# Optimization experiments

Measured on AMD Instinct MI355X. Metric: run time of the kernel, lower is better.

Reference implementation:

```python
import jax, jax.numpy as jnp
import numpy as np

CODEBOOK_SIZE = 1024
EMB_DIM = 64


def setup_inputs() -> dict:
    key = jax.random.key(0)
    k1, k2 = jax.random.split(key)
    z = jax.random.normal(k1, (4, EMB_DIM, 32, 32, 32), dtype=jnp.float32)
    embedding = jax.random.normal(k2, (CODEBOOK_SIZE, EMB_DIM), dtype=jnp.float32)
    return {"z": z, "embedding": embedding}


def reference(z, embedding):
    # z: [b, c, h, w, d], embedding: [K, c]
    b, c, h, w, d = z.shape
    K = embedding.shape[0]
    # flatten to [N, c] with channels last (matches permute(0,2,3,4,1).reshape)
    zf = jnp.transpose(z, (0, 2, 3, 4, 1)).reshape(-1, c)
    # squared L2 distance to each codebook entry: ||z||^2 - 2 z.e + ||e||^2
    dist = (
        jnp.sum(zf * zf, axis=1, keepdims=True)
        - 2.0 * zf @ embedding.T
        + jnp.sum(embedding * embedding, axis=1)[None, :]
    )  # [N, K]
    min_encoding_indices = jnp.argmin(dist, axis=1)  # [N]
    # one-hot @ embedding == gather (same math, no NxK materialization)
    z_q = embedding[min_encoding_indices]  # [N, c]
    z_q = jnp.transpose(z_q.reshape(b, h, w, d, c), (0, 4, 1, 2, 3))
    # straight-through estimator
    z_q = z + jax.lax.stop_gradient(z_q - z)
    # perplexity from mean one-hot occupancy
    n_tokens = zf.shape[0]
    e_mean = jnp.bincount(min_encoding_indices, length=K).astype(zf.dtype) / n_tokens
    perplexity = jnp.exp(-jnp.sum(e_mean * jnp.log(e_mean + 1e-10)))
    loss = jnp.asarray(0.0, dtype=z.dtype)
    return (
        z_q,
        loss,
        perplexity,
        min_encoding_indices.reshape(b, h, w, d),
        jnp.mean(dist),
    )
```

## Files before the change

kernel.cpp:

```cpp
#include <hip/hip_runtime.h>

#define CH     64
#define KC     1024
#define SP     32768
#define NBATCH 4
#define NTOK   (NBATCH * SP)
#define MTOK   64
#define SZZ    68
#define ECH    256
#define SZEB   72
#define CAP    16
#define MARGIN 3.0f

#define OFF_ZQ   0
#define OFF_LOSS (NBATCH * CH * SP)
#define OFF_PERP (OFF_LOSS + 1)
#define OFF_IDX  (OFF_PERP + 1)
#define OFF_MEAN (OFF_IDX + NTOK)


typedef __attribute__((ext_vector_type(8))) short  s16x8;
typedef __attribute__((ext_vector_type(4))) float  f32x4;

__device__ __forceinline__ unsigned short f2bf(float f) {
    unsigned int u = __float_as_uint(f);
    return (unsigned short)((u + 0x7fffu + ((u >> 16) & 1u)) >> 16);
}

__device__ __forceinline__ float exact_dist(const float* zrow,
                                            const float* __restrict__ emb,
                                            const float* enl, int c) {
    const float4* er = (const float4*)(emb + (size_t)c * CH);
    float a0 = 0.f, a1 = 0.f, a2 = 0.f, a3 = 0.f;
#pragma unroll
    for (int j = 0; j < 16; ++j) {
        float4 e4 = er[j];
        a0 = fmaf(zrow[4 * j + 0], e4.x, a0);
        a1 = fmaf(zrow[4 * j + 1], e4.y, a1);
        a2 = fmaf(zrow[4 * j + 2], e4.z, a2);
        a3 = fmaf(zrow[4 * j + 3], e4.w, a3);
    }
    return enl[c] - 2.f * ((a0 + a1) + (a2 + a3));
}

__global__ __launch_bounds__(256) void prep(const float* __restrict__ e,
                                            int* __restrict__ hist,
                                            float* __restrict__ sums,
                                            float* __restrict__ sum_zc,
                                            float* __restrict__ sum_ec,
                                            float* __restrict__ enorm,
                                            unsigned short* __restrict__ eb) {
    const int tid = threadIdx.x;
    const int bk = blockIdx.x;
    if (bk < 4) {
        int k = bk * 256 + tid;
        const float4* row = (const float4*)(e + (size_t)k * CH);
        float n = 0.f;
#pragma unroll
        for (int j = 0; j < CH / 4; ++j) {
            float4 v = row[j];
            n += v.x * v.x + v.y * v.y + v.z * v.z + v.w * v.w;
        }
        enorm[k] = n;
    } else if (bk == 4) {
        if (tid == 0) sums[0] = 0.f;
        if (tid < 64) sum_zc[tid] = 0.f;
        __shared__ float ls1[256];
        __shared__ float r2[4];
        int c = tid & 63;
        int strip = tid >> 6;
        float s1 = 0.f, s2 = 0.f;
        for (int k = strip * 256; k < strip * 256 + 256; ++k) {
            float v = e[k * CH + c];
            s1 += v;
            s2 = fmaf(v, v, s2);
        }
        ls1[tid] = s1;
        for (int off = 32; off; off >>= 1) s2 += __shfl_down(s2, off);
        if ((tid & 63) == 0) r2[tid >> 6] = s2;
        __syncthreads();
        if (strip == 0) sum_ec[c] = ls1[c] + ls1[64 + c] + ls1[128 + c] + ls1[192 + c];
        if (tid == 0) sums[1] = r2[0] + r2[1] + r2[2] + r2[3];
    } else if (bk < 9) {
        hist[(bk - 5) * 256 + tid] = 0;
    } else {
        int base = (bk - 9) * 16384;
        for (int j = 0; j < 64; ++j) {
            int i = base + tid + j * 256;
            eb[i] = f2bf(e[i]);
        }
    }
}

__global__ __launch_bounds__(256, 2) void vq_main(const float* __restrict__ z,
                                                  const float* __restrict__ emb,
                                                  const unsigned short* __restrict__ eb,
                                                  const float* __restrict__ enorm,
                                                  float* __restrict__ out,
                                                  int* __restrict__ hist,
                                                  float* __restrict__ sums,
                                                  float* __restrict__ sum_zc) {
    __shared__ float zl[MTOK * SZZ];
    __shared__ unsigned short ebl[ECH * SZEB];
    __shared__ float enorm_l[KC];
    __shared__ float dmin_l[MTOK];
    __shared__ float zs1[256], zs2[256];
    __shared__ int   cand[MTOK][CAP];
    __shared__ int   ccnt[MTOK];
    __shared__ int   fi[MTOK];

    const int tid = threadIdx.x;
    const int w = tid >> 6;
    const int lane = tid & 63;
    const int n15 = lane & 15;
    const int q = lane >> 4;
    const int t0 = blockIdx.x * MTOK;
    const int bb = t0 >> 15;
    const int s0 = t0 & (SP - 1);

    {
        const float* zbase = z + ((size_t)bb * CH) * SP + s0;
#pragma unroll
        for (int j = 0; j < 4; ++j) {
            int idx = tid + j * 256;
            int c = idx >> 4;
            int tq = idx & 15;
            float4 v = *(const float4*)(zbase + (size_t)c * SP + tq * 4);
            zl[(4 * tq + 0) * SZZ + c] = v.x;
            zl[(4 * tq + 1) * SZZ + c] = v.y;
            zl[(4 * tq + 2) * SZZ + c] = v.z;
            zl[(4 * tq + 3) * SZZ + c] = v.w;
        }
#pragma unroll
        for (int j = 0; j < 4; ++j) enorm_l[tid + j * 256] = enorm[tid + j * 256];
        if (tid < MTOK) ccnt[tid] = 0;
    }
    __syncthreads();

    s16x8 A0, A1;
    {
        const float* zrow = &zl[(w * 16 + n15) * SZZ];
        float4 za = *(const float4*)(zrow + q * 8);
        float4 zb = *(const float4*)(zrow + q * 8 + 4);
        float4 zc = *(const float4*)(zrow + 32 + q * 8);
        float4 zd = *(const float4*)(zrow + 32 + q * 8 + 4);
        A0[0] = (short)f2bf(za.x); A0[1] = (short)f2bf(za.y);
        A0[2] = (short)f2bf(za.z); A0[3] = (short)f2bf(za.w);
        A0[4] = (short)f2bf(zb.x); A0[5] = (short)f2bf(zb.y);
        A0[6] = (short)f2bf(zb.z); A0[7] = (short)f2bf(zb.w);
        A1[0] = (short)f2bf(zc.x); A1[1] = (short)f2bf(zc.y);
        A1[2] = (short)f2bf(zc.z); A1[3] = (short)f2bf(zc.w);
        A1[4] = (short)f2bf(zd.x); A1[5] = (short)f2bf(zd.y);
        A1[6] = (short)f2bf(zd.z); A1[7] = (short)f2bf(zd.w);
    }
    const unsigned short* ebq = ebl + (size_t)n15 * SZEB + q * 8;

    float bmin[4] = {3.4e38f, 3.4e38f, 3.4e38f, 3.4e38f};
    for (int ch = 0; ch < 4; ++ch) {
        __syncthreads();
#pragma unroll
        for (int rep = 0; rep < 8; ++rep) {
            int i = tid + rep * 256;
            int row = i >> 3, j = i & 7;
            ((float4*)&ebl[row * SZEB])[j] =
                ((const float4*)(eb + (size_t)(ch * ECH + row) * CH))[j];
        }
        __syncthreads();
        for (int ct = 0; ct < 16; ++ct) {
            const unsigned short* p = ebq + ct * 16 * SZEB;
            s16x8 B0 = *(const s16x8*)p;
            s16x8 B1 = *(const s16x8*)(p + 32);
            f32x4 acc = {0.f, 0.f, 0.f, 0.f};
            acc = __builtin_amdgcn_mfma_f32_16x16x32_bf16(A0, B0, acc, 0, 0, 0);
            acc = __builtin_amdgcn_mfma_f32_16x16x32_bf16(A1, B1, acc, 0, 0, 0);
            float en = enorm_l[ch * ECH + ct * 16 + n15];
#pragma unroll
            for (int r = 0; r < 4; ++r) {
                float d = fmaf(-2.f, acc[r], en);
                bmin[r] = fminf(bmin[r], d);
            }
        }
    }
#pragma unroll
    for (int off = 1; off < 16; off <<= 1)
#pragma unroll
        for (int r = 0; r < 4; ++r)
            bmin[r] = fminf(bmin[r], __shfl_xor(bmin[r], off));
    if (n15 == 0)
#pragma unroll
        for (int r = 0; r < 4; ++r) dmin_l[w * 16 + 4 * q + r] = bmin[r];
    __syncthreads();

    float thr[4];
#pragma unroll
    for (int r = 0; r < 4; ++r) thr[r] = dmin_l[w * 16 + 4 * q + r] + MARGIN;
    for (int cc = 0; cc < 4; ++cc) {
        int ch = (cc == 0) ? 3 : (cc - 1);
        if (cc) {
            __syncthreads();
#pragma unroll
            for (int rep = 0; rep < 8; ++rep) {
                int i = tid + rep * 256;
                int row = i >> 3, j = i & 7;
                ((float4*)&ebl[row * SZEB])[j] =
                    ((const float4*)(eb + (size_t)(ch * ECH + row) * CH))[j];
            }
            __syncthreads();
        }
        for (int ct = 0; ct < 16; ++ct) {
            const unsigned short* p = ebq + ct * 16 * SZEB;
            s16x8 B0 = *(const s16x8*)p;
            s16x8 B1 = *(const s16x8*)(p + 32);
            f32x4 acc = {0.f, 0.f, 0.f, 0.f};
            acc = __builtin_amdgcn_mfma_f32_16x16x32_bf16(A0, B0, acc, 0, 0, 0);
            acc = __builtin_amdgcn_mfma_f32_16x16x32_bf16(A1, B1, acc, 0, 0, 0);
            float en = enorm_l[ch * ECH + ct * 16 + n15];
#pragma unroll
            for (int r = 0; r < 4; ++r) {
                float d = fmaf(-2.f, acc[r], en);
                if (d <= thr[r]) {
                    int t = w * 16 + 4 * q + r;
                    int pos = atomicAdd(&ccnt[t], 1);
                    if (pos < CAP) cand[t][pos] = ch * ECH + ct * 16 + n15;
                }
            }
        }
    }
    __syncthreads();

    if (tid < MTOK) {
        int t = tid;
        const float* zrow = &zl[t * SZZ];
        int cnt = ccnt[t];
        float best = 3.4e38f;
        int bi = 0;
        if (cnt <= CAP) {
            for (int j = 0; j < cnt; ++j) {
                int c = cand[t][j];
                float d = exact_dist(zrow, emb, enorm_l, c);
                if (d < best || (d == best && c < bi)) { best = d; bi = c; }
            }
        } else {
            for (int c = 0; c < KC; ++c) {
                float d = exact_dist(zrow, emb, enorm_l, c);
                if (d < best) { best = d; bi = c; }
            }
        }
        fi[t] = bi;
        out[OFF_IDX + t0 + t] = (float)bi;
        atomicAdd(&hist[bi], 1);
    }
    __syncthreads();

#pragma unroll
    for (int j = 0; j < 16; ++j) {
        int idx = tid + j * 256;
        int c = idx >> 6;
        int t = idx & 63;
        int code = fi[t];
        float ev = emb[(size_t)code * CH + c];
        float zv = zl[t * SZZ + c];
        out[OFF_ZQ + ((size_t)bb * CH + c) * SP + s0 + t] = zv + (ev - zv);
    }

    {
        int c = tid >> 2, qq = tid & 3;
        float s1 = 0.f, s2 = 0.f;
        for (int tt = 0; tt < 16; ++tt) {
            float v = zl[(qq * 16 + tt) * SZZ + c];
            s1 += v;
            s2 = fmaf(v, v, s2);
        }
        zs1[tid] = s1;
        zs2[tid] = s2;
    }
    __syncthreads();
    if (tid < 64) {
        float a = zs1[4 * tid] + zs1[4 * tid + 1] + zs1[4 * tid + 2] + zs1[4 * tid + 3];
        atomicAdd(&sum_zc[tid], a);
        float bsum = zs2[4 * tid] + zs2[4 * tid + 1] + zs2[4 * tid + 2] + zs2[4 * tid + 3];
        for (int off = 32; off; off >>= 1) bsum += __shfl_down(bsum, off);
        if (tid == 0) atomicAdd(&sums[0], bsum);
    }
}

__global__ __launch_bounds__(1024) void finalize(const int* __restrict__ hist,
                                                 const float* __restrict__ sums,
                                                 const float* __restrict__ sum_zc,
                                                 const float* __restrict__ sum_ec,
                                                 float* __restrict__ out) {
    __shared__ float red[1024];
    int k = threadIdx.x;
    float p = (float)hist[k] * (1.0f / (float)NTOK);
    red[k] = p * logf(p + 1e-10f);
    __syncthreads();
    for (int off = 512; off; off >>= 1) {
        if (k < off) red[k] += red[k + off];
        __syncthreads();
    }
    if (k == 0) {
        out[OFF_PERP] = expf(-red[0]);
        out[OFF_LOSS] = 0.f;
        double dot = 0.0;
        for (int c = 0; c < CH; ++c) dot += (double)sum_zc[c] * (double)sum_ec[c];
        double mean = ((double)KC * (double)sums[0] + (double)NTOK * (double)sums[1] - 2.0 * dot)
                      / ((double)NTOK * (double)KC);
        out[OFF_MEAN] = (float)mean;
    }
}

extern "C" void kernel_launch(void* const* d_in, const int* in_sizes, int n_in,
                              void* d_out, int out_size, void* d_ws, size_t ws_size,
                              hipStream_t stream) {
    const float* z   = (const float*)d_in[0];
    const float* emb = (const float*)d_in[1];
    float* out = (float*)d_out;

    int*            hist   = (int*)d_ws;
    float*          sums   = (float*)d_ws + 1024;
    float*          sum_zc = (float*)d_ws + 1026;
    float*          sum_ec = (float*)d_ws + 1090;
    float*          enorm  = (float*)d_ws + 1154;
    unsigned short* eb     = (unsigned short*)((int*)d_ws + 4096);

    prep<<<13, 256, 0, stream>>>(emb, hist, sums, sum_zc, sum_ec, enorm, eb);
    vq_main<<<NTOK / MTOK, 256, 0, stream>>>(z, emb, eb, enorm, out, hist, sums, sum_zc);
    finalize<<<1, 1024, 0, stream>>>(hist, sums, sum_zc, sum_ec, out);
}
```

Before: 227.7 us.

## Enlarge token tile, fuse codebook prep and finalize into the main kernel

Each block now handles 256 tokens instead of 64. Each wave keeps four bf16 A-fragments in registers and reuses every codebook B-fragment across them, so codebook LDS traffic per token drops. The separate prep and finalize kernels are removed: each block computes codebook norms and bf16 conversion itself, and the last block, chosen with an atomic ticket, computes perplexity and the mean distance. The exact rescoring and z_q write read z back from global into registers. The z sums for the mean are now taken from bf16-rounded values, which lowers their precision, and every block repeats the codebook norm computation.

```diff
diff --git a/kernel.cpp b/kernel.cpp
--- a/kernel.cpp
+++ b/kernel.cpp
@@ -5,11 +5,12 @@
 #define SP     32768
 #define NBATCH 4
 #define NTOK   (NBATCH * SP)
-#define MTOK   64
-#define SZZ    68
-#define ECH    256
-#define SZEB   72
-#define CAP    16
+#define MTOK   256
+#define NBLK   (NTOK / MTOK)
+#define SZB    72
+#define ECH    128
+#define NCH    (KC / ECH)
+#define CAP    12
 #define MARGIN 3.0f
 
 #define OFF_ZQ   0
@@ -18,6 +19,7 @@
 #define OFF_IDX  (OFF_PERP + 1)
 #define OFF_MEAN (OFF_IDX + NTOK)
 
+#define WS_WORDS 1100
 
 typedef __attribute__((ext_vector_type(8))) short  s16x8;
 typedef __attribute__((ext_vector_type(4))) float  f32x4;
@@ -27,87 +29,27 @@
     return (unsigned short)((u + 0x7fffu + ((u >> 16) & 1u)) >> 16);
 }
 
-__device__ __forceinline__ float exact_dist(const float* zrow,
-                                            const float* __restrict__ emb,
-                                            const float* enl, int c) {
-    const float4* er = (const float4*)(emb + (size_t)c * CH);
-    float a0 = 0.f, a1 = 0.f, a2 = 0.f, a3 = 0.f;
-#pragma unroll
-    for (int j = 0; j < 16; ++j) {
-        float4 e4 = er[j];
-        a0 = fmaf(zrow[4 * j + 0], e4.x, a0);
-        a1 = fmaf(zrow[4 * j + 1], e4.y, a1);
-        a2 = fmaf(zrow[4 * j + 2], e4.z, a2);
-        a3 = fmaf(zrow[4 * j + 3], e4.w, a3);
-    }
-    return enl[c] - 2.f * ((a0 + a1) + (a2 + a3));
-}
-
-__global__ __launch_bounds__(256) void prep(const float* __restrict__ e,
-                                            int* __restrict__ hist,
-                                            float* __restrict__ sums,
-                                            float* __restrict__ sum_zc,
-                                            float* __restrict__ sum_ec,
-                                            float* __restrict__ enorm,
-                                            unsigned short* __restrict__ eb) {
-    const int tid = threadIdx.x;
-    const int bk = blockIdx.x;
-    if (bk < 4) {
-        int k = bk * 256 + tid;
-        const float4* row = (const float4*)(e + (size_t)k * CH);
-        float n = 0.f;
-#pragma unroll
-        for (int j = 0; j < CH / 4; ++j) {
-            float4 v = row[j];
-            n += v.x * v.x + v.y * v.y + v.z * v.z + v.w * v.w;
-        }
-        enorm[k] = n;
-    } else if (bk == 4) {
-        if (tid == 0) sums[0] = 0.f;
-        if (tid < 64) sum_zc[tid] = 0.f;
-        __shared__ float ls1[256];
-        __shared__ float r2[4];
-        int c = tid & 63;
-        int strip = tid >> 6;
-        float s1 = 0.f, s2 = 0.f;
-        for (int k = strip * 256; k < strip * 256 + 256; ++k) {
-            float v = e[k * CH + c];
-            s1 += v;
-            s2 = fmaf(v, v, s2);
-        }
-        ls1[tid] = s1;
-        for (int off = 32; off; off >>= 1) s2 += __shfl_down(s2, off);
-        if ((tid & 63) == 0) r2[tid >> 6] = s2;
-        __syncthreads();
-        if (strip == 0) sum_ec[c] = ls1[c] + ls1[64 + c] + ls1[128 + c] + ls1[192 + c];
-        if (tid == 0) sums[1] = r2[0] + r2[1] + r2[2] + r2[3];
-    } else if (bk < 9) {
-        hist[(bk - 5) * 256 + tid] = 0;
-    } else {
-        int base = (bk - 9) * 16384;
-        for (int j = 0; j < 64; ++j) {
-            int i = base + tid + j * 256;
-            eb[i] = f2bf(e[i]);
-        }
-    }
+__global__ void init_ws(int* ws) {
+    for (int i = threadIdx.x; i < WS_WORDS; i += 256) ws[i] = 0;
 }
 
 __global__ __launch_bounds__(256, 2) void vq_main(const float* __restrict__ z,
                                                   const float* __restrict__ emb,
-                                                  const unsigned short* __restrict__ eb,
-                                                  const float* __restrict__ enorm,
                                                   float* __restrict__ out,
                                                   int* __restrict__ hist,
                                                   float* __restrict__ sums,
+                                                  int* __restrict__ ticket,
                                                   float* __restrict__ sum_zc) {
-    __shared__ float zl[MTOK * SZZ];
-    __shared__ unsigned short ebl[ECH * SZEB];
+    __shared__ unsigned short zl[MTOK * SZB];
+    __shared__ unsigned short ebl[ECH * SZB];
     __shared__ float enorm_l[KC];
     __shared__ float dmin_l[MTOK];
-    __shared__ float zs1[256], zs2[256];
     __shared__ int   cand[MTOK][CAP];
     __shared__ int   ccnt[MTOK];
-    __shared__ int   fi[MTOK];
+    __shared__ int   lastf;
+
+    float* red  = (float*)&cand[0][0];
+    float* red2 = (float*)ccnt;
 
     const int tid = threadIdx.x;
     const int w = tid >> 6;
@@ -121,191 +63,267 @@
     {
         const float* zbase = z + ((size_t)bb * CH) * SP + s0;
 #pragma unroll
-        for (int j = 0; j < 4; ++j) {
+        for (int j = 0; j < 16; ++j) {
             int idx = tid + j * 256;
-            int c = idx >> 4;
-            int tq = idx & 15;
+            int c = idx >> 6;
+            int tq = idx & 63;
             float4 v = *(const float4*)(zbase + (size_t)c * SP + tq * 4);
-            zl[(4 * tq + 0) * SZZ + c] = v.x;
-            zl[(4 * tq + 1) * SZZ + c] = v.y;
-            zl[(4 * tq + 2) * SZZ + c] = v.z;
-            zl[(4 * tq + 3) * SZZ + c] = v.w;
-        }
-#pragma unroll
-        for (int j = 0; j < 4; ++j) enorm_l[tid + j * 256] = enorm[tid + j * 256];
-        if (tid < MTOK) ccnt[tid] = 0;
-    }
-    __syncthreads();
-
-    s16x8 A0, A1;
-    {
-        const float* zrow = &zl[(w * 16 + n15) * SZZ];
-        float4 za = *(const float4*)(zrow + q * 8);
-        float4 zb = *(const float4*)(zrow + q * 8 + 4);
-        float4 zc = *(const float4*)(zrow + 32 + q * 8);
-        float4 zd = *(const float4*)(zrow + 32 + q * 8 + 4);
-        A0[0] = (short)f2bf(za.x); A0[1] = (short)f2bf(za.y);
-        A0[2] = (short)f2bf(za.z); A0[3] = (short)f2bf(za.w);
-        A0[4] = (short)f2bf(zb.x); A0[5] = (short)f2bf(zb.y);
-        A0[6] = (short)f2bf(zb.z); A0[7] = (short)f2bf(zb.w);
-        A1[0] = (short)f2bf(zc.x); A1[1] = (short)f2bf(zc.y);
-        A1[2] = (short)f2bf(zc.z); A1[3] = (short)f2bf(zc.w);
-        A1[4] = (short)f2bf(zd.x); A1[5] = (short)f2bf(zd.y);
-        A1[6] = (short)f2bf(zd.z); A1[7] = (short)f2bf(zd.w);
-    }
-    const unsigned short* ebq = ebl + (size_t)n15 * SZEB + q * 8;
-
-    float bmin[4] = {3.4e38f, 3.4e38f, 3.4e38f, 3.4e38f};
-    for (int ch = 0; ch < 4; ++ch) {
+            zl[(4 * tq + 0) * SZB + c] = f2bf(v.x);
+            zl[(4 * tq + 1) * SZB + c] = f2bf(v.y);
+            zl[(4 * tq + 2) * SZB + c] = f2bf(v.z);
+            zl[(4 * tq + 3) * SZB + c] = f2bf(v.w);
+        }
+    }
+#pragma unroll
+    for (int m = 0; m < 4; ++m) {
+        int code = tid + m * 256;
+        const float4* row = (const float4*)(emb + (size_t)code * CH);
+        float n = 0.f;
+#pragma unroll
+        for (int j = 0; j < CH / 4; ++j) {
+            float4 v = row[j];
+            n += v.x * v.x + v.y * v.y + v.z * v.z + v.w * v.w;
+        }
+        enorm_l[code] = n;
+    }
+    ccnt[tid] = 0;
+    __syncthreads();
+
+    s16x8 A0[4], A1[4];
+#pragma unroll
+    for (int p = 0; p < 4; ++p) {
+        int row = w * 64 + p * 16 + n15;
+        A0[p] = *(const s16x8*)&zl[row * SZB + q * 8];
+        A1[p] = *(const s16x8*)&zl[row * SZB + 32 + q * 8];
+    }
+
+    const float4* ef4 = (const float4*)emb;
+
+    float bmin[16];
+#pragma unroll
+    for (int s = 0; s < 16; ++s) bmin[s] = 3.4e38f;
+
+    for (int ch = 0; ch < NCH; ++ch) {
         __syncthreads();
 #pragma unroll
         for (int rep = 0; rep < 8; ++rep) {
             int i = tid + rep * 256;
-            int row = i >> 3, j = i & 7;
-            ((float4*)&ebl[row * SZEB])[j] =
-                ((const float4*)(eb + (size_t)(ch * ECH + row) * CH))[j];
-        }
-        __syncthreads();
-        for (int ct = 0; ct < 16; ++ct) {
-            const unsigned short* p = ebq + ct * 16 * SZEB;
+            int code = i >> 4, kq = i & 15;
+            float4 v = ef4[(size_t)(ch * ECH + code) * 16 + kq];
+            ushort4 pk = make_ushort4(f2bf(v.x), f2bf(v.y), f2bf(v.z), f2bf(v.w));
+            *(ushort4*)&ebl[code * SZB + kq * 4] = pk;
+        }
+        __syncthreads();
+        for (int ct = 0; ct < 8; ++ct) {
+            const unsigned short* p = &ebl[(ct * 16 + n15) * SZB + q * 8];
             s16x8 B0 = *(const s16x8*)p;
             s16x8 B1 = *(const s16x8*)(p + 32);
-            f32x4 acc = {0.f, 0.f, 0.f, 0.f};
-            acc = __builtin_amdgcn_mfma_f32_16x16x32_bf16(A0, B0, acc, 0, 0, 0);
-            acc = __builtin_amdgcn_mfma_f32_16x16x32_bf16(A1, B1, acc, 0, 0, 0);
             float en = enorm_l[ch * ECH + ct * 16 + n15];
 #pragma unroll
-            for (int r = 0; r < 4; ++r) {
-                float d = fmaf(-2.f, acc[r], en);
-                bmin[r] = fminf(bmin[r], d);
+            for (int pr = 0; pr < 4; ++pr) {
+                f32x4 acc = {0.f, 0.f, 0.f, 0.f};
+                acc = __builtin_amdgcn_mfma_f32_16x16x32_bf16(A0[pr], B0, acc, 0, 0, 0);
+                acc = __builtin_amdgcn_mfma_f32_16x16x32_bf16(A1[pr], B1, acc, 0, 0, 0);
+#pragma unroll
+                for (int r = 0; r < 4; ++r) {
+                    float d = fmaf(-2.f, acc[r], en);
+                    bmin[pr * 4 + r] = fminf(bmin[pr * 4 + r], d);
+                }
             }
         }
     }
 #pragma unroll
     for (int off = 1; off < 16; off <<= 1)
 #pragma unroll
+        for (int s = 0; s < 16; ++s)
+            bmin[s] = fminf(bmin[s], __shfl_xor(bmin[s], off));
+    if (n15 == 0)
+#pragma unroll
+        for (int pr = 0; pr < 4; ++pr)
+#pragma unroll
+            for (int r = 0; r < 4; ++r)
+                dmin_l[w * 64 + pr * 16 + 4 * q + r] = bmin[pr * 4 + r];
+    __syncthreads();
+
+    float thr[16];
+#pragma unroll
+    for (int pr = 0; pr < 4; ++pr)
+#pragma unroll
         for (int r = 0; r < 4; ++r)
-            bmin[r] = fminf(bmin[r], __shfl_xor(bmin[r], off));
-    if (n15 == 0)
-#pragma unroll
-        for (int r = 0; r < 4; ++r) dmin_l[w * 16 + 4 * q + r] = bmin[r];
-    __syncthreads();
-
-    float thr[4];
-#pragma unroll
-    for (int r = 0; r < 4; ++r) thr[r] = dmin_l[w * 16 + 4 * q + r] + MARGIN;
-    for (int cc = 0; cc < 4; ++cc) {
-        int ch = (cc == 0) ? 3 : (cc - 1);
+            thr[pr * 4 + r] = dmin_l[w * 64 + pr * 16 + 4 * q + r] + MARGIN;
+    for (int cc = 0; cc < NCH; ++cc) {
+        int ch = (cc == 0) ? (NCH - 1) : (cc - 1);
         if (cc) {
             __syncthreads();
 #pragma unroll
             for (int rep = 0; rep < 8; ++rep) {
                 int i = tid + rep * 256;
-                int row = i >> 3, j = i & 7;
-                ((float4*)&ebl[row * SZEB])[j] =
-                    ((const float4*)(eb + (size_t)(ch * ECH + row) * CH))[j];
+                int code = i >> 4, kq = i & 15;
+                float4 v = ef4[(size_t)(ch * ECH + code) * 16 + kq];
+                ushort4 pk = make_ushort4(f2bf(v.x), f2bf(v.y), f2bf(v.z), f2bf(v.w));
+                *(ushort4*)&ebl[code * SZB + kq * 4] = pk;
             }
             __syncthreads();
         }
-        for (int ct = 0; ct < 16; ++ct) {
-            const unsigned short* p = ebq + ct * 16 * SZEB;
+        for (int ct = 0; ct < 8; ++ct) {
+            const unsigned short* p = &ebl[(ct * 16 + n15) * SZB + q * 8];
             s16x8 B0 = *(const s16x8*)p;
             s16x8 B1 = *(const s16x8*)(p + 32);
-            f32x4 acc = {0.f, 0.f, 0.f, 0.f};
-            acc = __builtin_amdgcn_mfma_f32_16x16x32_bf16(A0, B0, acc, 0, 0, 0);
-            acc = __builtin_amdgcn_mfma_f32_16x16x32_bf16(A1, B1, acc, 0, 0, 0);
             float en = enorm_l[ch * ECH + ct * 16 + n15];
 #pragma unroll
-            for (int r = 0; r < 4; ++r) {
-                float d = fmaf(-2.f, acc[r], en);
-                if (d <= thr[r]) {
-                    int t = w * 16 + 4 * q + r;
-                    int pos = atomicAdd(&ccnt[t], 1);
-                    if (pos < CAP) cand[t][pos] = ch * ECH + ct * 16 + n15;
+            for (int pr = 0; pr < 4; ++pr) {
+                f32x4 acc = {0.f, 0.f, 0.f, 0.f};
+                acc = __builtin_amdgcn_mfma_f32_16x16x32_bf16(A0[pr], B0, acc, 0, 0, 0);
+                acc = __builtin_amdgcn_mfma_f32_16x16x32_bf16(A1[pr], B1, acc, 0, 0, 0);
+#pragma unroll
+                for (int r = 0; r < 4; ++r) {
+                    float d = fmaf(-2.f, acc[r], en);
+                    if (d <= thr[pr * 4 + r]) {
+                        int t = w * 64 + pr * 16 + 4 * q + r;
+                        int pos = atomicAdd(&ccnt[t], 1);
+                        if (pos < CAP) cand[t][pos] = ch * ECH + ct * 16 + n15;
+                    }
                 }
             }
         }
     }
     __syncthreads();
 
-    if (tid < MTOK) {
-        int t = tid;
-        const float* zrow = &zl[t * SZZ];
-        int cnt = ccnt[t];
+    float zzr[CH];
+    {
+        const float* zpt = z + ((size_t)bb * CH) * SP + s0 + tid;
+#pragma unroll
+        for (int c = 0; c < CH; ++c) zzr[c] = zpt[(size_t)c * SP];
+    }
+
+    int besti = 0;
+    {
+        int cnt = ccnt[tid];
         float best = 3.4e38f;
-        int bi = 0;
         if (cnt <= CAP) {
             for (int j = 0; j < cnt; ++j) {
-                int c = cand[t][j];
-                float d = exact_dist(zrow, emb, enorm_l, c);
-                if (d < best || (d == best && c < bi)) { best = d; bi = c; }
+                int c = cand[tid][j];
+                const float4* er = (const float4*)(emb + (size_t)c * CH);
+                float a0 = 0.f, a1 = 0.f, a2 = 0.f, a3 = 0.f;
+#pragma unroll
+                for (int j2 = 0; j2 < 16; ++j2) {
+                    float4 e4 = er[j2];
+                    a0 = fmaf(zzr[4 * j2 + 0], e4.x, a0);
+                    a1 = fmaf(zzr[4 * j2 + 1], e4.y, a1);
+                    a2 = fmaf(zzr[4 * j2 + 2], e4.z, a2);
+                    a3 = fmaf(zzr[4 * j2 + 3], e4.w, a3);
+                }
+                float d = enorm_l[c] - 2.f * ((a0 + a1) + (a2 + a3));
+                if (d < best || (d == best && c < besti)) { best = d; besti = c; }
             }
         } else {
             for (int c = 0; c < KC; ++c) {
-                float d = exact_dist(zrow, emb, enorm_l, c);
-                if (d < best) { best = d; bi = c; }
-            }
-        }
-        fi[t] = bi;
-        out[OFF_IDX + t0 + t] = (float)bi;
-        atomicAdd(&hist[bi], 1);
-    }
-    __syncthreads();
-
-#pragma unroll
-    for (int j = 0; j < 16; ++j) {
-        int idx = tid + j * 256;
-        int c = idx >> 6;
-        int t = idx & 63;
-        int code = fi[t];
-        float ev = emb[(size_t)code * CH + c];
-        float zv = zl[t * SZZ + c];
-        out[OFF_ZQ + ((size_t)bb * CH + c) * SP + s0 + t] = zv + (ev - zv);
-    }
+                const float4* er = (const float4*)(emb + (size_t)c * CH);
+                float a0 = 0.f, a1 = 0.f, a2 = 0.f, a3 = 0.f;
+#pragma unroll
+                for (int j2 = 0; j2 < 16; ++j2) {
+                    float4 e4 = er[j2];
+                    a0 = fmaf(zzr[4 * j2 + 0], e4.x, a0);
+                    a1 = fmaf(zzr[4 * j2 + 1], e4.y, a1);
+                    a2 = fmaf(zzr[4 * j2 + 2], e4.z, a2);
+                    a3 = fmaf(zzr[4 * j2 + 3], e4.w, a3);
+                }
+                float d = enorm_l[c] - 2.f * ((a0 + a1) + (a2 + a3));
+                if (d < best) { best = d; besti = c; }
+            }
+        }
+    }
+    out[OFF_IDX + t0 + tid] = (float)besti;
+    atomicAdd(&hist[besti], 1);
+
+    {
+        const float4* eq = (const float4*)(emb + (size_t)besti * CH);
+        float* oq = out + OFF_ZQ + (size_t)bb * (CH * SP) + s0 + tid;
+#pragma unroll
+        for (int j = 0; j < CH / 4; ++j) {
+            float4 v = eq[j];
+            int c = 4 * j;
+            oq[(size_t)(c + 0) * SP] = zzr[c + 0] + (v.x - zzr[c + 0]);
+            oq[(size_t)(c + 1) * SP] = zzr[c + 1] + (v.y - zzr[c + 1]);
+            oq[(size_t)(c + 2) * SP] = zzr[c + 2] + (v.z - zzr[c + 2]);
+            oq[(size_t)(c + 3) * SP] = zzr[c + 3] + (v.w - zzr[c + 3]);
+        }
+    }
+    __syncthreads();
 
     {
         int c = tid >> 2, qq = tid & 3;
         float s1 = 0.f, s2 = 0.f;
-        for (int tt = 0; tt < 16; ++tt) {
-            float v = zl[(qq * 16 + tt) * SZZ + c];
+        for (int tt = 0; tt < 64; ++tt) {
+            unsigned int u = (unsigned int)zl[(qq * 64 + tt) * SZB + c] << 16;
+            float v = __uint_as_float(u);
             s1 += v;
             s2 = fmaf(v, v, s2);
         }
-        zs1[tid] = s1;
-        zs2[tid] = s2;
+        red[tid] = s1;
+        red2[tid] = s2;
     }
     __syncthreads();
     if (tid < 64) {
-        float a = zs1[4 * tid] + zs1[4 * tid + 1] + zs1[4 * tid + 2] + zs1[4 * tid + 3];
+        float a = red[4 * tid] + red[4 * tid + 1] + red[4 * tid + 2] + red[4 * tid + 3];
         atomicAdd(&sum_zc[tid], a);
-        float bsum = zs2[4 * tid] + zs2[4 * tid + 1] + zs2[4 * tid + 2] + zs2[4 * tid + 3];
-        for (int off = 32; off; off >>= 1) bsum += __shfl_down(bsum, off);
-        if (tid == 0) atomicAdd(&sums[0], bsum);
-    }
-}
-
-__global__ __launch_bounds__(1024) void finalize(const int* __restrict__ hist,
-                                                 const float* __restrict__ sums,
-                                                 const float* __restrict__ sum_zc,
-                                                 const float* __restrict__ sum_ec,
-                                                 float* __restrict__ out) {
-    __shared__ float red[1024];
-    int k = threadIdx.x;
-    float p = (float)hist[k] * (1.0f / (float)NTOK);
-    red[k] = p * logf(p + 1e-10f);
-    __syncthreads();
-    for (int off = 512; off; off >>= 1) {
-        if (k < off) red[k] += red[k + off];
-        __syncthreads();
-    }
-    if (k == 0) {
-        out[OFF_PERP] = expf(-red[0]);
-        out[OFF_LOSS] = 0.f;
-        double dot = 0.0;
-        for (int c = 0; c < CH; ++c) dot += (double)sum_zc[c] * (double)sum_ec[c];
-        double mean = ((double)KC * (double)sums[0] + (double)NTOK * (double)sums[1] - 2.0 * dot)
-                      / ((double)NTOK * (double)KC);
-        out[OFF_MEAN] = (float)mean;
+        float b2 = red2[4 * tid] + red2[4 * tid + 1] + red2[4 * tid + 2] + red2[4 * tid + 3];
+        for (int off = 32; off; off >>= 1) b2 += __shfl_down(b2, off);
+        if (tid == 0) atomicAdd(&sums[0], b2);
+    }
+
+    __threadfence();
+    __syncthreads();
+    if (tid == 0) lastf = (atomicAdd(ticket, 1) == NBLK - 1);
+    __syncthreads();
+    if (lastf) {
+        __threadfence();
+        {
+            int c = tid & 63, strip = tid >> 6;
+            float s1 = 0.f, s2 = 0.f;
+            for (int k = strip * 256; k < strip * 256 + 256; ++k) {
+                float v = emb[k * CH + c];
+                s1 += v;
+                s2 = fmaf(v, v, s2);
+            }
+            red[tid] = s1;
+            red2[tid] = s2;
+        }
+        __syncthreads();
+        if (tid < 64)
+            dmin_l[tid] = red[tid] + red[64 + tid] + red[128 + tid] + red[192 + tid];
+        for (int off = 128; off; off >>= 1) {
+            __syncthreads();
+            if (tid < off) red2[tid] += red2[tid + off];
+        }
+        __syncthreads();
+        float sum_e2 = red2[0];
+        {
+            float pl = 0.f;
+#pragma unroll
+            for (int m = 0; m < 4; ++m) {
+                int hv = atomicAdd(&hist[tid + m * 256], 0);
+                float p = (float)hv * (1.0f / (float)NTOK);
+                pl += p * logf(p + 1e-10f);
+            }
+            red[tid] = pl;
+        }
+        for (int off = 128; off; off >>= 1) {
+            __syncthreads();
+            if (tid < off) red[tid] += red[tid + off];
+        }
+        __syncthreads();
+        if (tid == 0) {
+            out[OFF_PERP] = expf(-red[0]);
+            out[OFF_LOSS] = 0.f;
+            float sz2 = atomicAdd(&sums[0], 0.f);
+            double dot = 0.0;
+            for (int c = 0; c < CH; ++c)
+                dot += (double)atomicAdd(&sum_zc[c], 0.f) * (double)dmin_l[c];
+            double mean = ((double)KC * (double)sz2 + (double)NTOK * (double)sum_e2
+                           - 2.0 * dot) / ((double)NTOK * (double)KC);
+            out[OFF_MEAN] = (float)mean;
+        }
     }
 }
 
@@ -316,14 +334,11 @@
     const float* emb = (const float*)d_in[1];
     float* out = (float*)d_out;
 
-    int*            hist   = (int*)d_ws;
-    float*          sums   = (float*)d_ws + 1024;
-    float*          sum_zc = (float*)d_ws + 1026;
-    float*          sum_ec = (float*)d_ws + 1090;
-    float*          enorm  = (float*)d_ws + 1154;
-    unsigned short* eb     = (unsigned short*)((int*)d_ws + 4096);
-
-    prep<<<13, 256, 0, stream>>>(emb, hist, sums, sum_zc, sum_ec, enorm, eb);
-    vq_main<<<NTOK / MTOK, 256, 0, stream>>>(z, emb, eb, enorm, out, hist, sums, sum_zc);
-    finalize<<<1, 1024, 0, stream>>>(hist, sums, sum_zc, sum_ec, out);
+    int*   hist   = (int*)d_ws;
+    float* sums   = (float*)d_ws + 1024;
+    int*   ticket = (int*)d_ws + 1025;
+    float* sum_zc = (float*)d_ws + 1026;
+
+    init_ws<<<1, 256, 0, stream>>>((int*)d_ws);
+    vq_main<<<NBLK, 256, 0, stream>>>(z, emb, out, hist, sums, ticket, sum_zc);
 }
```

Measured after the change: 576.5 us. 153% more time.
